# Kernel tuning notes

Hardware: AMD Instinct MI355X
Metric: run time of the kernel (lower is better)

## Reference

```python
import jax, jax.numpy as jnp
import numpy as np


def setup_inputs() -> dict:
    key = jax.random.key(0)
    ks = jax.random.split(key, 6)
    B, T, dim, H = 4, 4096, 2048, 16
    s = 0.02
    x = jax.random.normal(ks[0], (B, T, dim), jnp.float32)
    w_q = jax.random.normal(ks[1], (dim, dim), jnp.float32) * s
    w_k = jax.random.normal(ks[2], (dim, dim), jnp.float32) * s
    w_v = jax.random.normal(ks[3], (dim, dim), jnp.float32) * s
    w_o = jax.random.normal(ks[4], (dim, dim), jnp.float32) * s
    w_router = jax.random.normal(ks[5], (H, dim), jnp.float32) * s
    return {"x": x, "w_q": w_q, "w_k": w_k, "w_v": w_v, "w_o": w_o,
            "w_router": w_router, "top_k": 512}


def reference(x, w_q, w_k, w_v, w_o, w_router, top_k):
    B, T, dim = x.shape
    H = w_router.shape[0]
    hd = dim // H
    K = min(top_k, T)

    # router: per-head token scores [B, H, T] -> top-k indices [B, H, K]
    router_scores = jnp.einsum('btd,hd->bht', x, w_router)
    _, idx = jax.lax.top_k(router_scores, K)

    def proj(w):
        # [B, T, dim] -> [B, H, T, hd]
        return (x @ w.T).reshape(B, T, H, hd).transpose(0, 2, 1, 3)

    q, k, v = proj(w_q), proj(w_k), proj(w_v)

    gather = lambda t: jnp.take_along_axis(t, idx[..., None], axis=2)  # [B,H,K,hd]
    q_s, k_s, v_s = gather(q), gather(k), gather(v)

    scale = hd ** -0.5
    scores = jnp.einsum('bhkd,bhld->bhkl', q_s, k_s) * scale  # [B,H,K,K]
    # causal mask on ORIGINAL positions: query pos >= key pos
    can_attend = idx[..., :, None] >= idx[..., None, :]
    scores = jnp.where(can_attend, scores, -jnp.inf)
    attn = jax.nn.softmax(scores, axis=-1)
    out_s = jnp.einsum('bhkl,bhld->bhkd', attn, v_s)  # [B,H,K,hd]

    # scatter back into zeros at selected positions (indices unique per (b,h))
    out = jnp.zeros_like(q)
    bi = jnp.arange(B)[:, None, None]
    hi = jnp.arange(H)[None, :, None]
    out = out.at[bi, hi, idx].set(out_s)

    out = out.transpose(0, 2, 1, 3).reshape(B, T, dim)
    return out @ w_o.T
```

## Files before the change

kernel.cpp:

```cpp
#include <hip/hip_runtime.h>
#include <math.h>

#define BB 4
#define TT 4096
#define DD 2048
#define HH 16
#define HDIM 128
#define KSEL 512
#define NBH (BB*HH)

using short8  = __attribute__((ext_vector_type(8))) short;
using short4v = __attribute__((ext_vector_type(4))) short;
using f32x4   = __attribute__((ext_vector_type(4))) float;

__device__ __forceinline__ short f2bf(float f) {
  unsigned u = __float_as_uint(f);
  u += 0x7fffu + ((u >> 16) & 1u);
  return (short)(u >> 16);
}
__device__ __forceinline__ float bf2f(short s) {
  return __uint_as_float(((unsigned)(unsigned short)s) << 16);
}

__device__ __forceinline__ void gload16(const short* g, short* l) {
  __builtin_amdgcn_global_load_lds(
      (const __attribute__((address_space(1))) void*)g,
      (__attribute__((address_space(3))) void*)l, 16, 0, 0);
}

__global__ __launch_bounds__(256) void k_cvt_w(const float* __restrict__ wq,
    const float* __restrict__ wk, const float* __restrict__ wv,
    const float* __restrict__ wo, short* __restrict__ dst) {
  const int wsel = blockIdx.y;
  const float* s = (wsel == 0) ? wq : (wsel == 1) ? wk : (wsel == 2) ? wv : wo;
  size_t base = (size_t)blockIdx.x * 2048 + (size_t)threadIdx.x * 8;
  float4 a = *(const float4*)(s + base);
  float4 b = *(const float4*)(s + base + 4);
  short8 o;
  o[0] = f2bf(a.x); o[1] = f2bf(a.y); o[2] = f2bf(a.z); o[3] = f2bf(a.w);
  o[4] = f2bf(b.x); o[5] = f2bf(b.y); o[6] = f2bf(b.z); o[7] = f2bf(b.w);
  *(short8*)&dst[(size_t)wsel * 4194304 + base] = o;
}

__global__ __launch_bounds__(256) void k_router2(const float* __restrict__ x,
    const float* __restrict__ wr, float* __restrict__ part,
    short* __restrict__ xb, const int writeXb) {
  __shared__ __align__(16) float Xs[128][36];
  __shared__ __align__(16) float Ws[16][36];
  const int tb = blockIdx.x, kq = blockIdx.y;
  const int tid = threadIdx.x;
  const int row0 = tb * 128;
  const int sr8 = tid >> 3, sc8 = (tid & 7) * 4;
  const int tq = tid >> 2, hq = tid & 3;
  const int kbase = kq * 256;
  float acc[2][4];
#pragma unroll
  for (int i = 0; i < 2; ++i)
#pragma unroll
    for (int j = 0; j < 4; ++j) acc[i][j] = 0.f;
  float4 xr[4], wreg;
  {
#pragma unroll
    for (int p = 0; p < 4; ++p)
      xr[p] = *(const float4*)(x + (size_t)(row0 + sr8 + p * 32) * DD + kbase + sc8);
    if (tid < 128) wreg = *(const float4*)(wr + (size_t)(tid >> 3) * DD + kbase + (tid & 7) * 4);
  }
  for (int c = 0; c < 8; ++c) {
    if (c) __syncthreads();
#pragma unroll
    for (int p = 0; p < 4; ++p) {
      *(float4*)&Xs[sr8 + p * 32][sc8] = xr[p];
      if (writeXb) {
        short4v b4;
        b4[0] = f2bf(xr[p].x); b4[1] = f2bf(xr[p].y);
        b4[2] = f2bf(xr[p].z); b4[3] = f2bf(xr[p].w);
        *(short4v*)(xb + (size_t)(row0 + sr8 + p * 32) * DD + kbase + c * 32 + sc8) = b4;
      }
    }
    if (tid < 128) *(float4*)&Ws[tid >> 3][(tid & 7) * 4] = wreg;
    __syncthreads();
    if (c < 7) {
      const int k0 = kbase + (c + 1) * 32;
#pragma unroll
      for (int p = 0; p < 4; ++p)
        xr[p] = *(const float4*)(x + (size_t)(row0 + sr8 + p * 32) * DD + k0 + sc8);
      if (tid < 128) wreg = *(const float4*)(wr + (size_t)(tid >> 3) * DD + k0 + (tid & 7) * 4);
    }
#pragma unroll
    for (int k4 = 0; k4 < 8; ++k4) {
      float4 xv0 = *(const float4*)&Xs[tq][k4 * 4];
      float4 xv1 = *(const float4*)&Xs[tq + 64][k4 * 4];
#pragma unroll
      for (int j = 0; j < 4; ++j) {
        float4 wv4 = *(const float4*)&Ws[hq + j * 4][k4 * 4];
        acc[0][j] += xv0.x * wv4.x + xv0.y * wv4.y + xv0.z * wv4.z + xv0.w * wv4.w;
        acc[1][j] += xv1.x * wv4.x + xv1.y * wv4.y + xv1.z * wv4.z + xv1.w * wv4.w;
      }
    }
  }
#pragma unroll
  for (int i = 0; i < 2; ++i) {
    int tg = row0 + tq + i * 64;
    int b = tg >> 12, t = tg & (TT - 1);
#pragma unroll
    for (int j = 0; j < 4; ++j)
      part[((size_t)kq * NBH + (b * HH + hq + j * 4)) * TT + t] = acc[i][j];
  }
}

__global__ __launch_bounds__(256) void k_router_sum(const float* __restrict__ part,
                                                    float* __restrict__ scores) {
  size_t i = ((size_t)blockIdx.x * 256 + threadIdx.x) * 4;
  const size_t S = (size_t)NBH * TT;
  float4 s = *(const float4*)(part + i);
#pragma unroll
  for (int k = 1; k < 8; ++k) {
    float4 v = *(const float4*)(part + k * S + i);
    s.x += v.x; s.y += v.y; s.z += v.z; s.w += v.w;
  }
  *(float4*)(scores + i) = s;
}

__global__ __launch_bounds__(512) void k_topk(const float* __restrict__ scores,
                                              int* __restrict__ idx,
                                              int* __restrict__ inv) {
  __shared__ unsigned hist[256];
  __shared__ unsigned ssum[257];
  __shared__ unsigned wtot[8];
  __shared__ unsigned sh_b;
  const int bh = blockIdx.x, tid = threadIdx.x;
  const int lane = tid & 63, wv = tid >> 6;
  const float* sc = scores + (size_t)bh * TT;
  unsigned key[8];
  {
    float4 v0 = *(const float4*)(sc + tid * 8);
    float4 v1 = *(const float4*)(sc + tid * 8 + 4);
    float vs[8] = {v0.x, v0.y, v0.z, v0.w, v1.x, v1.y, v1.z, v1.w};
#pragma unroll
    for (int i = 0; i < 8; ++i) {
      unsigned u = __float_as_uint(vs[i]);
      key[i] = (u & 0x80000000u) ? ~u : (u | 0x80000000u);
    }
  }
  unsigned prefix = 0, need = KSEL;
  for (int shift = 24; shift >= 0; shift -= 8) {
    if (tid < 256) hist[tid] = 0;
    __syncthreads();
#pragma unroll
    for (int i = 0; i < 8; ++i) {
      bool m = (shift == 24) || ((key[i] >> (shift + 8)) == prefix);
      if (m) atomicAdd(&hist[(key[i] >> shift) & 255], 1u);
    }
    __syncthreads();
    if (wv == 0) {
      unsigned v0 = hist[lane * 4], v1 = hist[lane * 4 + 1];
      unsigned v2 = hist[lane * 4 + 2], v3 = hist[lane * 4 + 3];
      unsigned s3 = v3, s2 = v2 + s3, s1 = v1 + s2, s0 = v0 + s1;
      unsigned t = s0;
#pragma unroll
      for (int off = 1; off < 64; off <<= 1) {
        unsigned o = __shfl_down(t, off);
        if (lane + off < 64) t += o;
      }
      unsigned above = t - s0;
      ssum[lane * 4]     = s0 + above;
      ssum[lane * 4 + 1] = s1 + above;
      ssum[lane * 4 + 2] = s2 + above;
      ssum[lane * 4 + 3] = s3 + above;
      if (lane == 0) ssum[256] = 0;
    }
    __syncthreads();
    if (tid < 256) {
      if (ssum[tid] >= need && ssum[tid + 1] < need) sh_b = (unsigned)tid;
    }
    __syncthreads();
    unsigned bstar = sh_b;
    need -= ssum[bstar + 1];
    prefix = (shift == 24) ? bstar : ((prefix << 8) | bstar);
  }
  const unsigned thr = prefix;
  unsigned cgt = 0, ceq = 0;
#pragma unroll
  for (int i = 0; i < 8; ++i) { cgt += (key[i] > thr); ceq += (key[i] == thr); }
  unsigned packed = (cgt << 16) | ceq;
  unsigned inc = packed;
#pragma unroll
  for (int off = 1; off < 64; off <<= 1) {
    unsigned o = __shfl_up(inc, off);
    if (lane >= off) inc += o;
  }
  if (lane == 63) wtot[wv] = inc;
  __syncthreads();
  unsigned wbase = 0;
#pragma unroll
  for (int w2 = 0; w2 < 8; ++w2) wbase += (w2 < wv) ? wtot[w2] : 0u;
  unsigned base = wbase + inc - packed;
  unsigned gt_before = base >> 16, eq_before = base & 0xffffu;
  int* op = idx + bh * KSEL;
  int* invrow = inv + (size_t)bh * TT;
#pragma unroll
  for (int i = 0; i < 8; ++i) {
    bool isgt = key[i] > thr, iseq = key[i] == thr;
    bool sel = isgt || (iseq && eq_before < need);
    int pos = -1;
    if (sel) {
      pos = (int)(gt_before + (eq_before < need ? eq_before : need));
      op[pos] = tid * 8 + i;
    }
    invrow[tid * 8 + i] = pos;
    gt_before += isgt; eq_before += iseq;
  }
}

template <int AB>
__global__ __launch_bounds__(256, 2) void k_qkv_mfma(
    const float* __restrict__ x, const short* __restrict__ xb,
    const short* __restrict__ wqb, const short* __restrict__ wkb,
    const short* __restrict__ wvb, const int* __restrict__ idx,
    short* __restrict__ q_s, short* __restrict__ k_s, short* __restrict__ v_t) {
  __shared__ __align__(16) short As[64 * 64];
  __shared__ __align__(16) short Bs[3][128 * 64];
  __shared__ int tIdx[64];
  const int L = blockIdx.x;
  const int bh = (L & 7) * 8 + (L >> 6);
  const int rt = (L >> 3) & 7;
  const int b = bh >> 4, h = bh & 15;
  const int tid = threadIdx.x;
  if (tid < 64) tIdx[tid] = idx[bh * KSEL + rt * 64 + tid];
  __syncthreads();
  const int lane = tid & 63, w = tid >> 6;
  const int g = lane >> 4, r15 = lane & 15;
  const int lcol8 = lane >> 3, lslot = lane & 7;
  const float* aPtr = nullptr;
  const short* aSrc0 = nullptr; const short* aSrc1 = nullptr;
  int arow = 0, rm = 0;
  if constexpr (AB) {
    int rowA0 = w * 16 + lcol8;
    int rowA1 = rowA0 + 8;
    aSrc0 = xb + ((size_t)b * TT + tIdx[rowA0]) * DD + ((lslot ^ lcol8) << 3);
    aSrc1 = xb + ((size_t)b * TT + tIdx[rowA1]) * DD + ((lslot ^ lcol8) << 3);
  } else {
    arow = tid >> 2;
    rm = arow & 7;
    aPtr = x + ((size_t)b * TT + tIdx[arow]) * DD + (tid & 3) * 16;
  }
  f32x4 acc[4][6];
#pragma unroll
  for (int m = 0; m < 4; ++m)
#pragma unroll
    for (int n = 0; n < 6; ++n) acc[m][n] = (f32x4){0.f, 0.f, 0.f, 0.f};
  for (int k0 = 0; k0 < DD; k0 += 64) {
    __syncthreads();
    {
      if constexpr (AB) {
        gload16(aSrc0 + k0, &As[(w * 16) * 64]);
        gload16(aSrc1 + k0, &As[(w * 16 + 8) * 64]);
      } else {
        float4 a0 = *(const float4*)(aPtr + k0);
        float4 a1 = *(const float4*)(aPtr + k0 + 4);
        float4 a2 = *(const float4*)(aPtr + k0 + 8);
        float4 a3 = *(const float4*)(aPtr + k0 + 12);
        short8 p0, p1;
        p0[0] = f2bf(a0.x); p0[1] = f2bf(a0.y); p0[2] = f2bf(a0.z); p0[3] = f2bf(a0.w);
        p0[4] = f2bf(a1.x); p0[5] = f2bf(a1.y); p0[6] = f2bf(a1.z); p0[7] = f2bf(a1.w);
        p1[0] = f2bf(a2.x); p1[1] = f2bf(a2.y); p1[2] = f2bf(a2.z); p1[3] = f2bf(a2.w);
        p1[4] = f2bf(a3.x); p1[5] = f2bf(a3.y); p1[6] = f2bf(a3.z); p1[7] = f2bf(a3.w);
        int kq = tid & 3;
        *(short8*)&As[arow * 64 + ((2 * kq) ^ rm) * 8] = p0;
        *(short8*)&As[arow * 64 + ((2 * kq + 1) ^ rm) * 8] = p1;
      }
#pragma unroll
      for (int t = 0; t < 12; ++t) {
        int gi = w * 12 + t;
        int p = gi >> 4;
        int c0 = (gi & 15) << 3;
        int col = c0 + lcol8;
        const short* wsrc = (p == 0 ? wqb : p == 1 ? wkb : wvb)
                          + ((size_t)(h * HDIM + col)) * DD + k0 + ((lslot ^ (col & 7)) << 3);
        gload16(wsrc, &Bs[p][c0 * 64]);
      }
    }
    __syncthreads();
#pragma unroll
    for (int ks = 0; ks < 2; ++ks) {
      short8 af[4], bfr[6];
#pragma unroll
      for (int m = 0; m < 4; ++m) {
        int row = m * 16 + r15;
        af[m] = *(const short8*)&As[row * 64 + ((ks * 4 + g) ^ (row & 7)) * 8];
      }
#pragma unroll
      for (int n = 0; n < 6; ++n) {
        int nf = w * 6 + n;
        int colr = (nf & 7) * 16 + r15;
        bfr[n] = *(const short8*)&Bs[nf >> 3][colr * 64 + ((ks * 4 + g) ^ (colr & 7)) * 8];
      }
#pragma unroll
      for (int m = 0; m < 4; ++m)
#pragma unroll
        for (int n = 0; n < 6; ++n)
          acc[m][n] = __builtin_amdgcn_mfma_f32_16x16x32_bf16(af[m], bfr[n], acc[m][n], 0, 0, 0);
    }
  }
#pragma unroll
  for (int n = 0; n < 6; ++n) {
    int nf = w * 6 + n;
    int p = nf >> 3;
    int col = (nf & 7) * 16 + r15;
    if (p == 2) {
#pragma unroll
      for (int m = 0; m < 4; ++m) {
        short4v pk;
#pragma unroll
        for (int r = 0; r < 4; ++r) pk[r] = f2bf(acc[m][n][r]);
        *(short4v*)&v_t[((size_t)bh * HDIM + col) * KSEL + rt * 64 + m * 16 + g * 4] = pk;
      }
    } else {
      short* dp = (p == 0) ? q_s : k_s;
#pragma unroll
      for (int m = 0; m < 4; ++m) {
        int row0 = rt * 64 + m * 16 + g * 4;
#pragma unroll
        for (int r = 0; r < 4; ++r)
          dp[((size_t)bh * KSEL + row0 + r) * HDIM + col] = f2bf(acc[m][n][r]);
      }
    }
  }
}

__global__ __launch_bounds__(256) void k_attn_mfma(const short* __restrict__ q_s,
    const short* __restrict__ k_s, const short* __restrict__ v_t,
    short* __restrict__ out_s) {
  __shared__ __align__(16) short Ks[64 * 128];
  __shared__ __align__(16) short Vt[128 * 64];
  __shared__ __align__(16) short Pl[4 * 16 * 72];
  const int bh = blockIdx.x, qt = blockIdx.y;
  const int tid = threadIdx.x;
  const int w = tid >> 6, lane = tid & 63;
  const int g = lane >> 4, r15 = lane & 15;
  const size_t bhbase = (size_t)bh * KSEL * HDIM;
  const int r0 = qt * 64;
  const float scale = 0.08838834764831845f;

  short8 qf[4];
  {
    const short* qrow = q_s + bhbase + (size_t)(r0 + w * 16 + r15) * HDIM;
#pragma unroll
    for (int ks = 0; ks < 4; ++ks)
      qf[ks] = *(const short8*)(qrow + ks * 32 + g * 8);
  }
  f32x4 o[8];
#pragma unroll
  for (int n = 0; n < 8; ++n) o[n] = (f32x4){0.f, 0.f, 0.f, 0.f};
  float mrow[4] = {-INFINITY, -INFINITY, -INFINITY, -INFINITY};
  float lrow[4] = {0.f, 0.f, 0.f, 0.f};

  short* myP = &Pl[w * 16 * 72];
  const int kl16 = lane >> 4, ks16 = lane & 15;
  const int vl8 = lane >> 3, vs8 = lane & 7;

  for (int kt = 0; kt <= qt; ++kt) {
    int l0 = kt * 64;
    __syncthreads();
    {
#pragma unroll
      for (int t = 0; t < 4; ++t) {
        int gi = w * 4 + t;
        int kr0 = gi * 4;
        int key = kr0 + kl16;
        const short* ksrc = k_s + bhbase + (size_t)(l0 + key) * HDIM + ((ks16 ^ (key & 7)) << 3);
        gload16(ksrc, &Ks[kr0 * 128]);
        int d0 = gi * 8;
        int d = d0 + vl8;
        const short* vsrc = v_t + ((size_t)bh * HDIM + d) * KSEL + l0 + ((vs8 ^ (d & 7)) << 3);
        gload16(vsrc, &Vt[d0 * 64]);
      }
    }
    __syncthreads();

    f32x4 s[4];
#pragma unroll
    for (int n = 0; n < 4; ++n) s[n] = (f32x4){0.f, 0.f, 0.f, 0.f};
#pragma unroll
    for (int ks = 0; ks < 4; ++ks) {
#pragma unroll
      for (int n = 0; n < 4; ++n) {
        int row = n * 16 + r15;
        short8 kf = *(const short8*)&Ks[row * 128 + ((ks * 4 + g) ^ (r15 & 7)) * 8];
        s[n] = __builtin_amdgcn_mfma_f32_16x16x32_bf16(qf[ks], kf, s[n], 0, 0, 0);
      }
    }

    const bool diag = (kt == qt);
    float sv[4][4];
#pragma unroll
    for (int n = 0; n < 4; ++n) {
      int key = kt * 64 + n * 16 + r15;
#pragma unroll
      for (int r = 0; r < 4; ++r) {
        float xv = s[n][r] * scale;
        int qrow = r0 + w * 16 + g * 4 + r;
        sv[n][r] = (diag && key > qrow) ? -INFINITY : xv;
      }
    }
    float corr[4];
#pragma unroll
    for (int r = 0; r < 4; ++r) {
      float tm = fmaxf(fmaxf(sv[0][r], sv[1][r]), fmaxf(sv[2][r], sv[3][r]));
#pragma unroll
      for (int off = 8; off; off >>= 1) tm = fmaxf(tm, __shfl_xor(tm, off));
      float newm = fmaxf(mrow[r], tm);
      corr[r] = __expf(mrow[r] - newm);
      mrow[r] = newm;
      float ps = 0.f;
#pragma unroll
      for (int n = 0; n < 4; ++n) {
        float pv = __expf(sv[n][r] - newm);
        sv[n][r] = pv;
        ps += pv;
      }
#pragma unroll
      for (int off = 8; off; off >>= 1) ps += __shfl_xor(ps, off);
      lrow[r] = lrow[r] * corr[r] + ps;
    }
    f32x4 corrv = {corr[0], corr[1], corr[2], corr[3]};
#pragma unroll
    for (int n = 0; n < 4; ++n)
#pragma unroll
      for (int r = 0; r < 4; ++r)
        myP[(g * 4 + r) * 72 + n * 16 + r15] = f2bf(sv[n][r]);
#pragma unroll
    for (int n = 0; n < 8; ++n) o[n] *= corrv;

    short8 pf[2];
#pragma unroll
    for (int ks = 0; ks < 2; ++ks)
      pf[ks] = *(const short8*)&myP[r15 * 72 + ks * 32 + g * 8];
#pragma unroll
    for (int ks = 0; ks < 2; ++ks)
#pragma unroll
      for (int n2 = 0; n2 < 8; ++n2) {
        int row = n2 * 16 + r15;
        short8 vf = *(const short8*)&Vt[row * 64 + ((ks * 4 + g) ^ (r15 & 7)) * 8];
        o[n2] = __builtin_amdgcn_mfma_f32_16x16x32_bf16(pf[ks], vf, o[n2], 0, 0, 0);
      }
  }

  float inv[4];
#pragma unroll
  for (int r = 0; r < 4; ++r) inv[r] = 1.f / lrow[r];
#pragma unroll
  for (int n2 = 0; n2 < 8; ++n2) {
#pragma unroll
    for (int r = 0; r < 4; ++r) {
      int qrow = r0 + w * 16 + g * 4 + r;
      out_s[bhbase + (size_t)qrow * HDIM + n2 * 16 + r15] = f2bf(o[n2][r] * inv[r]);
    }
  }
}

__global__ __launch_bounds__(256) void k_oproj_p1(
    const short* __restrict__ out_s_b, const short* __restrict__ wob,
    short* __restrict__ P) {
  __shared__ __align__(16) short As[128 * 64];
  __shared__ __align__(16) short Bs[128 * 64];
  const int h = blockIdx.x, rt = blockIdx.y, ct = blockIdx.z;
  const int tid = threadIdx.x;
  const int lane = tid & 63, wid = tid >> 6;
  const int wr = wid >> 1, wc = wid & 1;
  const int l8 = lane >> 3, s8 = lane & 7;
  f32x4 acc[4][4];
#pragma unroll
  for (int m = 0; m < 4; ++m)
#pragma unroll
    for (int n = 0; n < 4; ++n) acc[m][n] = (f32x4){0.f, 0.f, 0.f, 0.f};
  const int r15 = lane & 15, g = lane >> 4;
#pragma unroll
  for (int k0 = 0; k0 < HDIM; k0 += 64) {
    __syncthreads();
    {
#pragma unroll
      for (int t = 0; t < 4; ++t) {
        int gi = wid * 4 + t;
        int r0 = gi * 8;
        int row = r0 + l8;
        const short* asrc = out_s_b + ((size_t)h * KSEL + rt * 128 + row) * HDIM + k0
                          + ((s8 ^ (row & 7)) << 3);
        gload16(asrc, &As[r0 * 64]);
        const short* bsrc = wob + ((size_t)(ct * 128 + row)) * DD + h * HDIM + k0
                          + ((s8 ^ (row & 7)) << 3);
        gload16(bsrc, &Bs[r0 * 64]);
      }
    }
    __syncthreads();
#pragma unroll
    for (int ks = 0; ks < 2; ++ks) {
      short8 af[4], bfr[4];
#pragma unroll
      for (int m = 0; m < 4; ++m) {
        int row = wr * 64 + m * 16 + r15;
        int chunk = (ks * 4 + g) ^ (row & 7);
        af[m] = *(const short8*)&As[row * 64 + chunk * 8];
      }
#pragma unroll
      for (int n = 0; n < 4; ++n) {
        int col = wc * 64 + n * 16 + r15;
        int chunk = (ks * 4 + g) ^ (col & 7);
        bfr[n] = *(const short8*)&Bs[col * 64 + chunk * 8];
      }
#pragma unroll
      for (int m = 0; m < 4; ++m)
#pragma unroll
        for (int n = 0; n < 4; ++n)
          acc[m][n] = __builtin_amdgcn_mfma_f32_16x16x32_bf16(af[m], bfr[n], acc[m][n], 0, 0, 0);
    }
  }
#pragma unroll
  for (int m = 0; m < 4; ++m) {
#pragma unroll
    for (int r = 0; r < 4; ++r) {
      int row = rt * 128 + wr * 64 + m * 16 + g * 4 + r;
#pragma unroll
      for (int n = 0; n < 4; ++n) {
        int col = ct * 128 + wc * 64 + n * 16 + r15;
        P[((size_t)h * KSEL + row) * DD + col] = f2bf(acc[m][n][r]);
      }
    }
  }
}

__global__ __launch_bounds__(256) void k_oproj_p2(const short* __restrict__ P,
    const int* __restrict__ inv_b, float* __restrict__ out_b) {
  const int t = blockIdx.x, tid = threadIdx.x;
  const int c0 = tid * 8;
  float acc[8] = {0.f, 0.f, 0.f, 0.f, 0.f, 0.f, 0.f, 0.f};
#pragma unroll
  for (int h = 0; h < HH; ++h) {
    int k = inv_b[h * TT + t];
    if (k >= 0) {
      short8 pv = *(const short8*)&P[((size_t)h * KSEL + k) * DD + c0];
#pragma unroll
      for (int e = 0; e < 8; ++e) acc[e] += bf2f(pv[e]);
    }
  }
  float4 o0 = {acc[0], acc[1], acc[2], acc[3]};
  float4 o1 = {acc[4], acc[5], acc[6], acc[7]};
  *(float4*)&out_b[(size_t)t * DD + c0] = o0;
  *(float4*)&out_b[(size_t)t * DD + c0 + 4] = o1;
}

extern "C" void kernel_launch(void* const* d_in, const int* in_sizes, int n_in,
                              void* d_out, int out_size, void* d_ws, size_t ws_size,
                              hipStream_t stream) {
  (void)in_sizes; (void)n_in; (void)out_size;
  const float* x  = (const float*)d_in[0];
  const float* wq = (const float*)d_in[1];
  const float* wk = (const float*)d_in[2];
  const float* wv = (const float*)d_in[3];
  const float* wo = (const float*)d_in[4];
  const float* wr = (const float*)d_in[5];
  float* out = (float*)d_out;

  char* ws = (char*)d_ws;
  float* scores = (float*)ws;
  int*   idx    = (int*)(ws + 1048576);
  short* wqb    = (short*)(ws + 1179648);
  short* wkb    = wqb + 4194304;
  short* wvb    = wkb + 4194304;
  short* wob    = wvb + 4194304;
  short* out_s  = wob + 4194304;
  int*   inv    = (int*)((char*)out_s + 8388608);
  short* P      = (short*)((char*)inv + 1048576);
  short* q_s    = P;
  short* k_s    = P + 4194304;
  short* v_t    = P + 8388608;
  float* part   = (float*)P;
  const size_t NEED_XB = 144834560ULL;
  const int big = (ws_size >= NEED_XB) ? 1 : 0;
  short* xb = big ? (short*)(ws + 77725696) : (short*)ws;

  k_cvt_w<<<dim3(2048, 4), 256, 0, stream>>>(wq, wk, wv, wo, wqb);
  k_router2<<<dim3(128, 8), 256, 0, stream>>>(x, wr, part, xb, big);
  k_router_sum<<<256, 256, 0, stream>>>(part, scores);
  k_topk<<<NBH, 512, 0, stream>>>(scores, idx, inv);
  if (big)
    k_qkv_mfma<1><<<512, 256, 0, stream>>>(x, xb, wqb, wkb, wvb, idx, q_s, k_s, v_t);
  else
    k_qkv_mfma<0><<<512, 256, 0, stream>>>(x, xb, wqb, wkb, wvb, idx, q_s, k_s, v_t);
  k_attn_mfma<<<dim3(NBH, KSEL / 64), 256, 0, stream>>>(q_s, k_s, v_t, out_s);
  for (int b = 0; b < BB; ++b) {
    k_oproj_p1<<<dim3(HH, KSEL / 128, DD / 128), 256, 0, stream>>>(
        out_s + (size_t)b * HH * KSEL * HDIM, wob, P);
    k_oproj_p2<<<TT, 256, 0, stream>>>(
        P, inv + (size_t)b * HH * TT, out + (size_t)b * TT * DD);
  }
}
```

Before: 281.8 us.

## Split QKV GEMM column tiles in half and double-buffer LDS loads

The gathered QKV projection kernel now splits each head's 128 output columns into two 64-column halves, which doubles the grid from 512 to 1024 blocks. Each block keeps half as many accumulators. Shared-memory tiles are double-buffered so the next k-slice is loaded while MFMAs run on the current one, leaving one barrier per iteration instead of two. The aim is more parallelism across CUs and less global load latency exposed. In exchange, the gathered A rows are read twice, once per half, and LDS use per block stays about the same.

```diff
diff --git a/kernel.cpp b/kernel.cpp
--- a/kernel.cpp
+++ b/kernel.cpp
@@ -218,12 +218,14 @@
     const short* __restrict__ wqb, const short* __restrict__ wkb,
     const short* __restrict__ wvb, const int* __restrict__ idx,
     short* __restrict__ q_s, short* __restrict__ k_s, short* __restrict__ v_t) {
-  __shared__ __align__(16) short As[64 * 64];
-  __shared__ __align__(16) short Bs[3][128 * 64];
+  __shared__ __align__(16) short As[2][64 * 64];
+  __shared__ __align__(16) short Bs[2][3][64 * 64];
   __shared__ int tIdx[64];
   const int L = blockIdx.x;
-  const int bh = (L & 7) * 8 + (L >> 6);
+  const int xcd = L & 7;
+  const int bh = xcd * 8 + (L >> 7);
   const int rt = (L >> 3) & 7;
+  const int ch = (L >> 6) & 1;
   const int b = bh >> 4, h = bh & 15;
   const int tid = threadIdx.x;
   if (tid < 64) tIdx[tid] = idx[bh * KSEL + rt * 64 + tid];
@@ -236,84 +238,93 @@
   int arow = 0, rm = 0;
   if constexpr (AB) {
     int rowA0 = w * 16 + lcol8;
-    int rowA1 = rowA0 + 8;
     aSrc0 = xb + ((size_t)b * TT + tIdx[rowA0]) * DD + ((lslot ^ lcol8) << 3);
-    aSrc1 = xb + ((size_t)b * TT + tIdx[rowA1]) * DD + ((lslot ^ lcol8) << 3);
+    aSrc1 = xb + ((size_t)b * TT + tIdx[rowA0 + 8]) * DD + ((lslot ^ lcol8) << 3);
   } else {
     arow = tid >> 2;
     rm = arow & 7;
     aPtr = x + ((size_t)b * TT + tIdx[arow]) * DD + (tid & 3) * 16;
   }
-  f32x4 acc[4][6];
+  const short* wbase[3] = {wqb, wkb, wvb};
+  f32x4 acc[4][3];
 #pragma unroll
   for (int m = 0; m < 4; ++m)
 #pragma unroll
-    for (int n = 0; n < 6; ++n) acc[m][n] = (f32x4){0.f, 0.f, 0.f, 0.f};
+    for (int n = 0; n < 3; ++n) acc[m][n] = (f32x4){0.f, 0.f, 0.f, 0.f};
+
+#define STAGE(BUF, K0)                                                          \
+  {                                                                             \
+    if constexpr (AB) {                                                         \
+      gload16(aSrc0 + (K0), &As[BUF][(w * 16) * 64]);                           \
+      gload16(aSrc1 + (K0), &As[BUF][(w * 16 + 8) * 64]);                       \
+    } else {                                                                    \
+      float4 a0 = *(const float4*)(aPtr + (K0));                                \
+      float4 a1 = *(const float4*)(aPtr + (K0) + 4);                            \
+      float4 a2 = *(const float4*)(aPtr + (K0) + 8);                            \
+      float4 a3 = *(const float4*)(aPtr + (K0) + 12);                           \
+      short8 p0, p1;                                                            \
+      p0[0] = f2bf(a0.x); p0[1] = f2bf(a0.y); p0[2] = f2bf(a0.z); p0[3] = f2bf(a0.w); \
+      p0[4] = f2bf(a1.x); p0[5] = f2bf(a1.y); p0[6] = f2bf(a1.z); p0[7] = f2bf(a1.w); \
+      p1[0] = f2bf(a2.x); p1[1] = f2bf(a2.y); p1[2] = f2bf(a2.z); p1[3] = f2bf(a2.w); \
+      p1[4] = f2bf(a3.x); p1[5] = f2bf(a3.y); p1[6] = f2bf(a3.z); p1[7] = f2bf(a3.w); \
+      int kq = tid & 3;                                                         \
+      *(short8*)&As[BUF][arow * 64 + ((2 * kq) ^ rm) * 8] = p0;                 \
+      *(short8*)&As[BUF][arow * 64 + ((2 * kq + 1) ^ rm) * 8] = p1;             \
+    }                                                                           \
+    _Pragma("unroll")                                                           \
+    for (int t = 0; t < 6; ++t) {                                               \
+      int gi = w * 6 + t;                                                       \
+      int p = gi >> 3;                                                          \
+      int c0 = (gi & 7) << 3;                                                   \
+      int colg = ch * 64 + c0 + lcol8;                                          \
+      const short* wsrc = wbase[p] + ((size_t)(h * HDIM + colg)) * DD + (K0)    \
+                        + ((lslot ^ lcol8) << 3);                               \
+      gload16(wsrc, &Bs[BUF][p][c0 * 64]);                                      \
+    }                                                                           \
+  }
+
+  STAGE(0, 0);
+  __syncthreads();
+  int cur = 0;
   for (int k0 = 0; k0 < DD; k0 += 64) {
-    __syncthreads();
-    {
-      if constexpr (AB) {
-        gload16(aSrc0 + k0, &As[(w * 16) * 64]);
-        gload16(aSrc1 + k0, &As[(w * 16 + 8) * 64]);
-      } else {
-        float4 a0 = *(const float4*)(aPtr + k0);
-        float4 a1 = *(const float4*)(aPtr + k0 + 4);
-        float4 a2 = *(const float4*)(aPtr + k0 + 8);
-        float4 a3 = *(const float4*)(aPtr + k0 + 12);
-        short8 p0, p1;
-        p0[0] = f2bf(a0.x); p0[1] = f2bf(a0.y); p0[2] = f2bf(a0.z); p0[3] = f2bf(a0.w);
-        p0[4] = f2bf(a1.x); p0[5] = f2bf(a1.y); p0[6] = f2bf(a1.z); p0[7] = f2bf(a1.w);
-        p1[0] = f2bf(a2.x); p1[1] = f2bf(a2.y); p1[2] = f2bf(a2.z); p1[3] = f2bf(a2.w);
-        p1[4] = f2bf(a3.x); p1[5] = f2bf(a3.y); p1[6] = f2bf(a3.z); p1[7] = f2bf(a3.w);
-        int kq = tid & 3;
-        *(short8*)&As[arow * 64 + ((2 * kq) ^ rm) * 8] = p0;
-        *(short8*)&As[arow * 64 + ((2 * kq + 1) ^ rm) * 8] = p1;
-      }
-#pragma unroll
-      for (int t = 0; t < 12; ++t) {
-        int gi = w * 12 + t;
-        int p = gi >> 4;
-        int c0 = (gi & 15) << 3;
-        int col = c0 + lcol8;
-        const short* wsrc = (p == 0 ? wqb : p == 1 ? wkb : wvb)
-                          + ((size_t)(h * HDIM + col)) * DD + k0 + ((lslot ^ (col & 7)) << 3);
-        gload16(wsrc, &Bs[p][c0 * 64]);
-      }
-    }
-    __syncthreads();
+    if (k0 + 64 < DD) STAGE(cur ^ 1, k0 + 64);
 #pragma unroll
     for (int ks = 0; ks < 2; ++ks) {
-      short8 af[4], bfr[6];
+      short8 af[4], bfr[3];
 #pragma unroll
       for (int m = 0; m < 4; ++m) {
         int row = m * 16 + r15;
-        af[m] = *(const short8*)&As[row * 64 + ((ks * 4 + g) ^ (row & 7)) * 8];
-      }
-#pragma unroll
-      for (int n = 0; n < 6; ++n) {
-        int nf = w * 6 + n;
-        int colr = (nf & 7) * 16 + r15;
-        bfr[n] = *(const short8*)&Bs[nf >> 3][colr * 64 + ((ks * 4 + g) ^ (colr & 7)) * 8];
+        af[m] = *(const short8*)&As[cur][row * 64 + ((ks * 4 + g) ^ (row & 7)) * 8];
+      }
+#pragma unroll
+      for (int n = 0; n < 3; ++n) {
+        int nf = w * 3 + n;
+        int coll = (nf & 3) * 16 + r15;
+        bfr[n] = *(const short8*)&Bs[cur][nf >> 2][coll * 64 + ((ks * 4 + g) ^ (coll & 7)) * 8];
       }
 #pragma unroll
       for (int m = 0; m < 4; ++m)
 #pragma unroll
-        for (int n = 0; n < 6; ++n)
+        for (int n = 0; n < 3; ++n)
           acc[m][n] = __builtin_amdgcn_mfma_f32_16x16x32_bf16(af[m], bfr[n], acc[m][n], 0, 0, 0);
     }
-  }
-#pragma unroll
-  for (int n = 0; n < 6; ++n) {
-    int nf = w * 6 + n;
-    int p = nf >> 3;
-    int col = (nf & 7) * 16 + r15;
+    __syncthreads();
+    cur ^= 1;
+  }
+#undef STAGE
+
+#pragma unroll
+  for (int n = 0; n < 3; ++n) {
+    int nf = w * 3 + n;
+    int p = nf >> 2;
+    int colg = ch * 64 + (nf & 3) * 16 + r15;
     if (p == 2) {
 #pragma unroll
       for (int m = 0; m < 4; ++m) {
         short4v pk;
 #pragma unroll
         for (int r = 0; r < 4; ++r) pk[r] = f2bf(acc[m][n][r]);
-        *(short4v*)&v_t[((size_t)bh * HDIM + col) * KSEL + rt * 64 + m * 16 + g * 4] = pk;
+        *(short4v*)&v_t[((size_t)bh * HDIM + colg) * KSEL + rt * 64 + m * 16 + g * 4] = pk;
       }
     } else {
       short* dp = (p == 0) ? q_s : k_s;
@@ -322,7 +333,7 @@
         int row0 = rt * 64 + m * 16 + g * 4;
 #pragma unroll
         for (int r = 0; r < 4; ++r)
-          dp[((size_t)bh * KSEL + row0 + r) * HDIM + col] = f2bf(acc[m][n][r]);
+          dp[((size_t)bh * KSEL + row0 + r) * HDIM + colg] = f2bf(acc[m][n][r]);
       }
     }
   }
@@ -584,9 +595,9 @@
   k_router_sum<<<256, 256, 0, stream>>>(part, scores);
   k_topk<<<NBH, 512, 0, stream>>>(scores, idx, inv);
   if (big)
-    k_qkv_mfma<1><<<512, 256, 0, stream>>>(x, xb, wqb, wkb, wvb, idx, q_s, k_s, v_t);
+    k_qkv_mfma<1><<<1024, 256, 0, stream>>>(x, xb, wqb, wkb, wvb, idx, q_s, k_s, v_t);
   else
-    k_qkv_mfma<0><<<512, 256, 0, stream>>>(x, xb, wqb, wkb, wvb, idx, q_s, k_s, v_t);
+    k_qkv_mfma<0><<<1024, 256, 0, stream>>>(x, xb, wqb, wkb, wvb, idx, q_s, k_s, v_t);
   k_attn_mfma<<<dim3(NBH, KSEL / 64), 256, 0, stream>>>(q_s, k_s, v_t, out_s);
   for (int b = 0; b < BB; ++b) {
     k_oproj_p1<<<dim3(HH, KSEL / 128, DD / 128), 256, 0, stream>>>(
```

Measured after the change: 298.9 us. 6.1% more time.
